# Optimization experiments

Measured on AMD Instinct MI355X. Metric: run time of the kernel, lower is better.

Reference implementation:

```python
import jax, jax.numpy as jnp
import numpy as np

B, S, D = 2, 2048, 2048
H, KVH, HD = 16, 4, 128
I = 8192
EPS = 1e-6
SCALE = HD ** -0.5
NEG = -1e9


def rms_norm(x, w):
    xf = x.astype(jnp.float32)
    var = jnp.mean(xf * xf, axis=-1, keepdims=True)
    return (w * (xf * jax.lax.rsqrt(var + EPS)).astype(x.dtype))


def rope(x, cos_f, sin_f):
    # x: (B, h, S, HD); cos_f/sin_f: (B, 1, S, HD//2). Interleaved pairs.
    xp = x.reshape(*x.shape[:-1], HD // 2, 2)
    xr, xi = xp[..., 0], xp[..., 1]
    rr = cos_f * xr - sin_f * xi
    ri = sin_f * xr + cos_f * xi
    return jnp.stack([rr, ri], axis=-1).reshape(x.shape)


def setup_inputs() -> dict:
    key = jax.random.key(0)
    ks = jax.random.split(key, 12)
    inp = {
        "hidden_states": jax.random.normal(ks[0], (B, S, D), jnp.float32),
        "cos": jax.random.normal(ks[1], (B, S, HD), jnp.float32),
        "sin": jax.random.normal(ks[2], (B, S, HD), jnp.float32),
    }
    # additive causal mask (B,1,S,S)
    causal = jnp.tril(jnp.ones((S, S), jnp.bool_))
    inp["attention_mask"] = jnp.where(causal, 0.0, NEG).astype(jnp.float32)[None, None].repeat(B, 0)
    sc = 0.02
    inp["wq"] = jax.random.normal(ks[3], (H * HD, D), jnp.float32) * sc
    inp["wk"] = jax.random.normal(ks[4], (KVH * HD, D), jnp.float32) * sc
    inp["wv"] = jax.random.normal(ks[5], (KVH * HD, D), jnp.float32) * sc
    inp["wo"] = jax.random.normal(ks[6], (D, H * HD), jnp.float32) * sc
    inp["w_gate"] = jax.random.normal(ks[7], (I, D), jnp.float32) * sc
    inp["w_up"] = jax.random.normal(ks[8], (I, D), jnp.float32) * sc
    inp["w_down"] = jax.random.normal(ks[9], (D, I), jnp.float32) * sc
    inp["ln1_w"] = jnp.ones((D,), jnp.float32)
    inp["ln2_w"] = jnp.ones((D,), jnp.float32)
    return inp


def layer_fwd(hidden_states, cos, sin, attention_mask,
              wq, wk, wv, wo, w_gate, w_up, w_down, ln1_w, ln2_w):
    residual = hidden_states
    h = rms_norm(hidden_states, ln1_w)
    # projections
    q = jnp.einsum('bsd,ed->bse', h, wq).reshape(B, S, H, HD).transpose(0, 2, 1, 3)
    k = jnp.einsum('bsd,ed->bse', h, wk).reshape(B, S, KVH, HD).transpose(0, 2, 1, 3)
    v = jnp.einsum('bsd,ed->bse', h, wv).reshape(B, S, KVH, HD).transpose(0, 2, 1, 3)
    cos_f = cos[..., :HD // 2][:, None]  # (B,1,S,HD/2)
    sin_f = sin[..., :HD // 2][:, None]
    q = rope(q, cos_f, sin_f)
    k = rope(k, cos_f, sin_f)
    # GQA: repeat_interleave kv heads
    n_rep = H // KVH
    k = jnp.repeat(k, n_rep, axis=1)
    v = jnp.repeat(v, n_rep, axis=1)
    scores = jnp.einsum('bhqd,bhkd->bhqk', q, k) * SCALE + attention_mask
    probs = jax.nn.softmax(scores.astype(jnp.float32), axis=-1).astype(q.dtype)
    attn = jnp.einsum('bhqk,bhkd->bhqd', probs, v)
    attn = attn.transpose(0, 2, 1, 3).reshape(B, S, H * HD)
    attn_out = jnp.einsum('bse,de->bsd', attn, wo)
    h = residual + attn_out
    residual = h
    m = rms_norm(h, ln2_w)
    gate = jax.nn.silu(jnp.einsum('bsd,id->bsi', m, w_gate))
    up = jnp.einsum('bsd,id->bsi', m, w_up)
    mlp_out = jnp.einsum('bsi,di->bsd', gate * up, w_down)
    return residual + mlp_out


def reference(hidden_states, cos, sin, attention_mask,
              wq, wk, wv, wo, w_gate, w_up, w_down, ln1_w, ln2_w):
    return layer_fwd(hidden_states, cos, sin, attention_mask,
                     wq, wk, wv, wo, w_gate, w_up, w_down, ln1_w, ln2_w)
```

## Files before the change

### kernel.cpp

```cpp
#include <hip/hip_runtime.h>
#include <cstdint>
#include <cstddef>

typedef unsigned short u16;
typedef short bf16x8 __attribute__((ext_vector_type(8)));
typedef float floatx4 __attribute__((ext_vector_type(4)));

__device__ __forceinline__ float b2f(u16 u) {
    union { unsigned int i; float f; } v; v.i = ((unsigned int)u) << 16; return v.f;
}
__device__ __forceinline__ u16 f2b(float f) {
    union { float f; unsigned int i; } v; v.f = f;
    unsigned int u = v.i;
    unsigned int r = (u + 0x7fffu + ((u >> 16) & 1u)) >> 16;
    return (u16)r;
}

#define GLL16(gptr, lptr)                                                          \
    __builtin_amdgcn_global_load_lds(                                              \
        (__attribute__((address_space(1))) void*)(gptr),                           \
        (__attribute__((address_space(3))) void*)(lptr), 16, 0, 0)

#define BAR_LGKM() asm volatile("s_waitcnt lgkmcnt(0)\n\ts_barrier" ::: "memory")
#define WAIT_VM8_BAR() asm volatile("s_waitcnt vmcnt(8)\n\ts_barrier" ::: "memory")
#define WAIT_VM0_BAR() asm volatile("s_waitcnt vmcnt(0)\n\ts_barrier" ::: "memory")
#define VMW(n) asm volatile("s_waitcnt vmcnt(" #n ")" ::: "memory")
#define LGKM0() asm volatile("s_waitcnt lgkmcnt(0)" ::: "memory")

__global__ __launch_bounds__(256) void cvt_all(
    const float* __restrict__ wq, const float* __restrict__ wk,
    const float* __restrict__ wvp, const float* __restrict__ wo,
    const float* __restrict__ wg, const float* __restrict__ wu,
    const float* __restrict__ wd,
    u16* __restrict__ wqkv, u16* __restrict__ wob, u16* __restrict__ wgb,
    u16* __restrict__ wub, u16* __restrict__ wdb) {
    long v = (long)blockIdx.x * 256 + threadIdx.x;
    const float* s; u16* d; long o;
    if (v < 1048576)       { s = wq;  d = wqkv;           o = v; }
    else if (v < 1310720)  { s = wk;  d = wqkv + 4194304; o = v - 1048576; }
    else if (v < 1572864)  { s = wvp; d = wqkv + 5242880; o = v - 1310720; }
    else if (v < 2621440)  { s = wo;  d = wob;            o = v - 1572864; }
    else if (v < 6815744)  { s = wg;  d = wgb;            o = v - 2621440; }
    else if (v < 11010048) { s = wu;  d = wub;            o = v - 6815744; }
    else                   { s = wd;  d = wdb;            o = v - 11010048; }
    float4 x = ((const float4*)s)[o];
    u16 t[4] = { f2b(x.x), f2b(x.y), f2b(x.z), f2b(x.w) };
    ((ushort4*)d)[o] = *(const ushort4*)t;
}

__global__ __launch_bounds__(256) void rmsnorm_kernel(const float* __restrict__ x,
                                                      const float* __restrict__ w,
                                                      u16* __restrict__ out) {
    __shared__ float red[4];
    const int row = blockIdx.x;
    const float* xr = x + (size_t)row * 2048;
    const int d0 = threadIdx.x * 8;
    float4 a = *(const float4*)&xr[d0];
    float4 b = *(const float4*)&xr[d0 + 4];
    float s = a.x*a.x + a.y*a.y + a.z*a.z + a.w*a.w +
              b.x*b.x + b.y*b.y + b.z*b.z + b.w*b.w;
    #pragma unroll
    for (int m = 1; m < 64; m <<= 1) s += __shfl_xor(s, m);
    const int lane = threadIdx.x & 63, wv = threadIdx.x >> 6;
    if (lane == 0) red[wv] = s;
    __syncthreads();
    float tot = red[0] + red[1] + red[2] + red[3];
    float r = rsqrtf(tot * (1.0f / 2048.0f) + 1e-6f);
    const float* wp = w + d0;
    u16 o[8];
    o[0] = f2b(a.x * r * wp[0]); o[1] = f2b(a.y * r * wp[1]);
    o[2] = f2b(a.z * r * wp[2]); o[3] = f2b(a.w * r * wp[3]);
    o[4] = f2b(b.x * r * wp[4]); o[5] = f2b(b.y * r * wp[5]);
    o[6] = f2b(b.z * r * wp[6]); o[7] = f2b(b.w * r * wp[7]);
    *(bf16x8*)&out[(size_t)row * 2048 + d0] = *(const bf16x8*)o;
}

__global__ __launch_bounds__(256, 2) void gemm_bt(
    const u16* __restrict__ A, const u16* __restrict__ W,
    int M, int N, int K, int mode,
    u16* __restrict__ outb, float* __restrict__ outf,
    const float* __restrict__ res) {

    __shared__ __align__(16) u16 smA[2][128 * 64];
    __shared__ __align__(16) u16 smB[2][128 * 64];

    const int tid  = threadIdx.x;
    const int lane = tid & 63;
    const int c    = lane & 15;
    const int quad = lane >> 4;
    const int wv   = tid >> 6;
    const int wm   = (wv >> 1) * 64;
    const int wn   = (wv & 1) * 64;
    const int row0 = blockIdx.y * 128;
    const int col0 = blockIdx.x * 128;

    const u16* aB[4]; const u16* bB[4]; int lo[4];
    #pragma unroll
    for (int p = 0; p < 4; ++p) {
        int lin = p * 256 + tid, r = lin >> 3, g = lin & 7, sg = g ^ (r & 7);
        aB[p] = A + (size_t)(row0 + r) * K + sg * 8;
        bB[p] = W + (size_t)(col0 + r) * K + sg * 8;
        lo[p] = lin * 8;
    }
    #pragma unroll
    for (int p = 0; p < 4; ++p) { GLL16(aB[p], &smA[0][lo[p]]); GLL16(bB[p], &smB[0][lo[p]]); }

    floatx4 acc[4][4] = {};
    const int nk = K >> 6;
    for (int k = 0; k < nk; ++k) {
        BAR_LGKM();
        if (k + 1 < nk) {
            const int nb = (k + 1) & 1, ko = (k + 1) << 6;
            #pragma unroll
            for (int p = 0; p < 4; ++p) {
                GLL16(aB[p] + ko, &smA[nb][lo[p]]);
                GLL16(bB[p] + ko, &smB[nb][lo[p]]);
            }
            WAIT_VM8_BAR();
        } else {
            WAIT_VM0_BAR();
        }
        const u16* sA = smA[k & 1];
        const u16* sB = smB[k & 1];
        #pragma unroll
        for (int ks = 0; ks < 2; ++ks) {
            bf16x8 af[4], bfr[4];
            #pragma unroll
            for (int mi = 0; mi < 4; ++mi) {
                int r = wm + mi * 16 + c;
                int pos = (ks * 4 + quad) ^ (c & 7);
                af[mi] = *(const bf16x8*)&sA[r * 64 + pos * 8];
            }
            #pragma unroll
            for (int ni = 0; ni < 4; ++ni) {
                int r = wn + ni * 16 + c;
                int pos = (ks * 4 + quad) ^ (c & 7);
                bfr[ni] = *(const bf16x8*)&sB[r * 64 + pos * 8];
            }
            #pragma unroll
            for (int mi = 0; mi < 4; ++mi)
                #pragma unroll
                for (int ni = 0; ni < 4; ++ni)
                    acc[mi][ni] = __builtin_amdgcn_mfma_f32_16x16x32_bf16(
                        af[mi], bfr[ni], acc[mi][ni], 0, 0, 0);
        }
    }

    #pragma unroll
    for (int mi = 0; mi < 4; ++mi) {
        #pragma unroll
        for (int r = 0; r < 4; ++r) {
            int row = row0 + wm + mi * 16 + quad * 4 + r;
            #pragma unroll
            for (int ni = 0; ni < 4; ++ni) {
                int col = col0 + wn + ni * 16 + c;
                size_t idx = (size_t)row * N + col;
                float v = acc[mi][ni][r];
                if (mode == 0) outb[idx] = f2b(v);
                else           outf[idx] = v + res[idx];
            }
        }
    }
}

#define STAGE_G(buf, ko) { GLL16(gSrc0 + (ko), &smG[buf][guD0]); GLL16(gSrc1 + (ko), &smG[buf][guD1]); }
#define STAGE_U(buf, ko) { GLL16(uSrc0 + (ko), &smU[buf][guD0]); GLL16(uSrc1 + (ko), &smU[buf][guD1]); }
#define STAGE_A(buf, ko, j)                                                    \
    GLL16(aSrc + (size_t)(j) * 32 * 2048 + (ko), &smA[buf][aDst + (j) * 32 * 64])

#define READ_B()                                                               \
    _Pragma("unroll")                                                          \
    for (int ks = 0; ks < 2; ++ks)                                             \
        _Pragma("unroll")                                                      \
        for (int ni = 0; ni < 2; ++ni) {                                       \
            int r = wn + ni * 16 + c;                                          \
            int pos = (ks * 4 + quad) ^ (c & 7);                               \
            bg[ni][ks] = *(const bf16x8*)&sG[r * 64 + pos * 8];                \
            bu[ni][ks] = *(const bf16x8*)&sU[r * 64 + pos * 8];                \
        }

#define MLP_PH(ph, WAITCODE, READS_EXTRA, STAGE_STMT)                          \
    {                                                                          \
        WAITCODE;                                                              \
        __builtin_amdgcn_s_barrier();                                          \
        READS_EXTRA;                                                           \
        bf16x8 af[2][2];                                                       \
        _Pragma("unroll")                                                      \
        for (int mi = 0; mi < 2; ++mi)                                         \
            _Pragma("unroll")                                                  \
            for (int ks = 0; ks < 2; ++ks) {                                   \
                int r = wm + (ph) * 32 + mi * 16 + c;                          \
                int pos = (ks * 4 + quad) ^ (c & 7);                           \
                af[mi][ks] = *(const bf16x8*)&sA[r * 64 + pos * 8];            \
            }                                                                  \
        STAGE_STMT;                                                            \
        LGKM0();                                                               \
        __builtin_amdgcn_s_setprio(1);                                         \
        _Pragma("unroll")                                                      \
        for (int mi = 0; mi < 2; ++mi)                                         \
            _Pragma("unroll")                                                  \
            for (int ks = 0; ks < 2; ++ks)                                     \
                _Pragma("unroll")                                              \
                for (int ni = 0; ni < 2; ++ni) {                               \
                    ag[(ph) * 2 + mi][ni] = __builtin_amdgcn_mfma_f32_16x16x32_bf16( \
                        af[mi][ks], bg[ni][ks], ag[(ph) * 2 + mi][ni], 0, 0, 0);     \
                    au[(ph) * 2 + mi][ni] = __builtin_amdgcn_mfma_f32_16x16x32_bf16( \
                        af[mi][ks], bu[ni][ks], au[(ph) * 2 + mi][ni], 0, 0, 0);     \
                }                                                              \
        __builtin_amdgcn_s_setprio(0);                                         \
    }

__global__ __launch_bounds__(512, 2) void mlp_gateup4(
    const u16* __restrict__ A, const u16* __restrict__ Wg,
    const u16* __restrict__ Wu, u16* __restrict__ out) {

    __shared__ __align__(16) u16 smA[2][256 * 64];
    __shared__ __align__(16) u16 smG[2][128 * 64];
    __shared__ __align__(16) u16 smU[2][128 * 64];

    const int K = 2048;
    const int tid  = threadIdx.x;
    const int lane = tid & 63;
    const int c    = lane & 15;
    const int quad = lane >> 4;
    const int wv   = tid >> 6;
    const int wm   = (wv >> 2) * 128;
    const int wn   = (wv & 3) * 32;

    const int bid  = (int)blockIdx.x;
    const int orig = (bid & 7) * 128 + (bid >> 3);
    const int row0 = (orig & 15) * 256;
    const int col0 = (orig >> 4) * 128;

    const int rloc = tid >> 3, g = tid & 7;
    const int Rbase = (tid < 256) ? rloc : (96 + rloc);
    const int sgA = g ^ (rloc & 7);
    const u16* aSrc = A + (size_t)(row0 + Rbase) * K + sgA * 8;
    const int aDst = Rbase * 64 + g * 8;

    const u16* gSrc0; const u16* gSrc1; const u16* uSrc0; const u16* uSrc1;
    int guD0, guD1;
    {
        int lin = tid, r = lin >> 3, gg = lin & 7, sg = gg ^ (r & 7);
        gSrc0 = Wg + (size_t)(col0 + r) * K + sg * 8;
        uSrc0 = Wu + (size_t)(col0 + r) * K + sg * 8;
        guD0 = lin * 8;
        lin = 512 + tid; r = lin >> 3; gg = lin & 7; sg = gg ^ (r & 7);
        gSrc1 = Wg + (size_t)(col0 + r) * K + sg * 8;
        uSrc1 = Wu + (size_t)(col0 + r) * K + sg * 8;
        guD1 = lin * 8;
    }

    STAGE_G(0, 0); STAGE_U(0, 0);
    STAGE_A(0, 0, 0); STAGE_A(0, 0, 1); STAGE_A(0, 0, 2); STAGE_A(0, 0, 3);

    floatx4 ag[8][2] = {}, au[8][2] = {};
    const int nk = K >> 6;
    for (int k = 0; k < nk; ++k) {
        const int cur = k & 1, nb = cur ^ 1;
        const int ko = (k + 1) << 6;
        const u16* sA = smA[cur];
        const u16* sG = smG[cur];
        const u16* sU = smU[cur];
        bf16x8 bg[2][2], bu[2][2];

        if (k + 1 < nk) {
            MLP_PH(0, VMW(3), READ_B(),
                   { STAGE_G(nb, ko); STAGE_U(nb, ko); STAGE_A(nb, ko, 0); });
            MLP_PH(1, VMW(7), , STAGE_A(nb, ko, 1));
            MLP_PH(2, VMW(7), , STAGE_A(nb, ko, 2));
            MLP_PH(3, VMW(7), , STAGE_A(nb, ko, 3));
        } else {
            MLP_PH(0, VMW(3), READ_B(), );
            MLP_PH(1, VMW(2), , );
            MLP_PH(2, VMW(1), , );
            MLP_PH(3, VMW(0), , );
        }
    }

    #pragma unroll
    for (int mi = 0; mi < 8; ++mi) {
        #pragma unroll
        for (int r = 0; r < 4; ++r) {
            int row = row0 + wm + mi * 16 + quad * 4 + r;
            #pragma unroll
            for (int ni = 0; ni < 2; ++ni) {
                int col = col0 + wn + ni * 16 + c;
                float gv = ag[mi][ni][r];
                float uv = au[mi][ni][r];
                float sg_ = gv / (1.0f + __expf(-gv));
                out[(size_t)row * 8192 + col] = f2b(sg_ * uv);
            }
        }
    }
}

__global__ __launch_bounds__(256) void rope_kernel(u16* __restrict__ qkv,
                                                   const float* __restrict__ cs,
                                                   const float* __restrict__ sn) {
    const int t = blockIdx.x;
    const int hh = blockIdx.y * 4 + (threadIdx.x >> 6);
    const int j = threadIdx.x & 63;
    size_t base = (size_t)t * 3072 + (hh < 16 ? hh * 128 : 2048 + (hh - 16) * 128);
    float cf = cs[(size_t)t * 128 + j];
    float sf = sn[(size_t)t * 128 + j];
    ushort2 xv = *(ushort2*)&qkv[base + 2 * j];
    float xr = b2f(xv.x), xi = b2f(xv.y);
    ushort2 ov;
    ov.x = f2b(cf * xr - sf * xi);
    ov.y = f2b(sf * xr + cf * xi);
    *(ushort2*)&qkv[base + 2 * j] = ov;
}

__global__ __launch_bounds__(256) void transpose_v(const u16* __restrict__ qkv,
                                                   u16* __restrict__ vt) {
    __shared__ __align__(16) u16 T[64][136];
    const int bkv = blockIdx.x;
    const int st = blockIdx.y;
    const int b = bkv >> 2, kvh = bkv & 3;
    const int tid = threadIdx.x;
    #pragma unroll
    for (int it = 0; it < 4; ++it) {
        int lin = it * 256 + tid;
        int sr = lin >> 4, gr = lin & 15;
        bf16x8 v = *(const bf16x8*)&qkv[((size_t)(b * 2048 + st * 64 + sr)) * 3072 +
                                        2560 + kvh * 128 + gr * 8];
        *(bf16x8*)&T[sr][gr * 8] = v;
    }
    __syncthreads();
    #pragma unroll
    for (int it = 0; it < 4; ++it) {
        int lin = it * 256 + tid;
        int n = lin >> 3, sc = lin & 7;
        u16 tmp[8];
        #pragma unroll
        for (int j = 0; j < 8; ++j) tmp[j] = T[sc * 8 + j][n];
        *(bf16x8*)&vt[((size_t)(bkv * 128 + n)) * 2048 + st * 64 + sc * 8] =
            *(const bf16x8*)tmp;
    }
}

__global__ __launch_bounds__(256, 2) void attn_kernel(const u16* __restrict__ qkv,
                                                      const u16* __restrict__ vt,
                                                      u16* __restrict__ attnb) {
    __shared__ __align__(16) u16 sK[64 * 128];
    __shared__ __align__(16) u16 sV[128 * 64];
    __shared__ __align__(16) u16 sP[4][16 * 80];

    const int tid  = threadIdx.x;
    const int lane = tid & 63;
    const int c    = lane & 15;
    const int quad = lane >> 4;
    const int wv   = tid >> 6;

    const int qt  = 31 - (int)blockIdx.x;
    const int bh  = blockIdx.y;
    const int b   = bh >> 4;
    const int h   = bh & 15;
    const int kvh = h >> 2;

    const int qrow = qt * 64 + wv * 16 + c;
    const size_t qbase = ((size_t)(b * 2048 + qrow)) * 3072 + h * 128;
    bf16x8 qf[4];
    #pragma unroll
    for (int kk = 0; kk < 4; ++kk)
        qf[kk] = *(const bf16x8*)&qkv[qbase + kk * 32 + quad * 8];

    floatx4 o[8] = {};
    float m_[4], l_[4];
    #pragma unroll
    for (int r = 0; r < 4; ++r) { m_[r] = -__builtin_inff(); l_[r] = 0.0f; }

    const float SC = 0.08838834764831845f;

    for (int kt = 0; kt <= qt; ++kt) {
        const int kv0 = kt * 64;
        __syncthreads();
        #pragma unroll
        for (int p = 0; p < 4; ++p) {
            int lin = p * 256 + tid;
            {
                int r = lin >> 4, g = lin & 15;
                int sg = g ^ (r & 7);
                const u16* gk = qkv + ((size_t)(b * 2048 + kv0 + r)) * 3072 +
                                2048 + kvh * 128 + sg * 8;
                GLL16(gk, &sK[lin * 8]);
            }
            {
                int r = lin >> 3, g = lin & 7;
                int sg = g ^ (r & 7);
                const u16* gv = vt + ((size_t)((b * 4 + kvh) * 128 + r)) * 2048 +
                                kv0 + sg * 8;
                GLL16(gv, &sV[lin * 8]);
            }
        }
        __syncthreads();

        floatx4 s[4] = {};
        #pragma unroll
        for (int kk = 0; kk < 4; ++kk) {
            #pragma unroll
            for (int ct = 0; ct < 4; ++ct) {
                int rk = ct * 16 + c;
                int pos = (kk * 4 + quad) ^ (c & 7);
                bf16x8 kf = *(const bf16x8*)&sK[rk * 128 + pos * 8];
                s[ct] = __builtin_amdgcn_mfma_f32_16x16x32_bf16(qf[kk], kf, s[ct], 0, 0, 0);
            }
        }

        const int qloc = wv * 16 + quad * 4;
        #pragma unroll
        for (int ct = 0; ct < 4; ++ct) {
            #pragma unroll
            for (int r = 0; r < 4; ++r) {
                float v = s[ct][r] * SC;
                if (kt == qt && (ct * 16 + c) > (qloc + r)) v = -__builtin_inff();
                s[ct][r] = v;
            }
        }

        float alpha[4];
        #pragma unroll
        for (int r = 0; r < 4; ++r) {
            float rm = fmaxf(fmaxf(s[0][r], s[1][r]), fmaxf(s[2][r], s[3][r]));
            rm = fmaxf(rm, __shfl_xor(rm, 1));
            rm = fmaxf(rm, __shfl_xor(rm, 2));
            rm = fmaxf(rm, __shfl_xor(rm, 4));
            rm = fmaxf(rm, __shfl_xor(rm, 8));
            float mn = fmaxf(m_[r], rm);
            alpha[r] = __expf(m_[r] - mn);
            m_[r] = mn;
        }
        #pragma unroll
        for (int r = 0; r < 4; ++r) {
            float rs = 0.0f;
            #pragma unroll
            for (int ct = 0; ct < 4; ++ct) {
                float p = __expf(s[ct][r] - m_[r]);
                s[ct][r] = p;
                rs += p;
            }
            rs += __shfl_xor(rs, 1);
            rs += __shfl_xor(rs, 2);
            rs += __shfl_xor(rs, 4);
            rs += __shfl_xor(rs, 8);
            l_[r] = l_[r] * alpha[r] + rs;
        }

        u16* sp = &sP[wv][0];
        #pragma unroll
        for (int ct = 0; ct < 4; ++ct)
            #pragma unroll
            for (int r = 0; r < 4; ++r)
                sp[(quad * 4 + r) * 80 + ct * 16 + c] = f2b(s[ct][r]);

        #pragma unroll
        for (int nt = 0; nt < 8; ++nt)
            #pragma unroll
            for (int r = 0; r < 4; ++r)
                o[nt][r] *= alpha[r];

        #pragma unroll
        for (int ks2 = 0; ks2 < 2; ++ks2) {
            bf16x8 pa = *(const bf16x8*)&sp[c * 80 + ks2 * 32 + quad * 8];
            #pragma unroll
            for (int nt = 0; nt < 8; ++nt) {
                int rv = nt * 16 + c;
                int pos = (ks2 * 4 + quad) ^ (c & 7);
                bf16x8 vb = *(const bf16x8*)&sV[rv * 64 + pos * 8];
                o[nt] = __builtin_amdgcn_mfma_f32_16x16x32_bf16(pa, vb, o[nt], 0, 0, 0);
            }
        }
    }

    float inv[4];
    #pragma unroll
    for (int r = 0; r < 4; ++r) inv[r] = 1.0f / l_[r];
    #pragma unroll
    for (int nt = 0; nt < 8; ++nt) {
        #pragma unroll
        for (int r = 0; r < 4; ++r) {
            int row = qt * 64 + wv * 16 + quad * 4 + r;
            int col = h * 128 + nt * 16 + c;
            attnb[((size_t)(b * 2048 + row)) * 2048 + col] = f2b(o[nt][r] * inv[r]);
        }
    }
}

extern "C" void kernel_launch(void* const* d_in, const int* in_sizes, int n_in,
                              void* d_out, int out_size, void* d_ws, size_t ws_size,
                              hipStream_t stream) {
    const float* hidden = (const float*)d_in[0];
    const float* cosp   = (const float*)d_in[1];
    const float* sinp   = (const float*)d_in[2];
    const float* wq  = (const float*)d_in[4];
    const float* wk  = (const float*)d_in[5];
    const float* wvp = (const float*)d_in[6];
    const float* wo  = (const float*)d_in[7];
    const float* wg  = (const float*)d_in[8];
    const float* wu  = (const float*)d_in[9];
    const float* wd  = (const float*)d_in[10];
    const float* ln1 = (const float*)d_in[11];
    const float* ln2 = (const float*)d_in[12];
    float* outp = (float*)d_out;

    char* ws = (char*)d_ws;
    size_t off = 0;
    auto alloc = [&](size_t bytes) {
        void* p = ws + off;
        off += (bytes + 255) & ~(size_t)255;
        return p;
    };
    u16* wqkv_b  = (u16*)alloc((size_t)3072 * 2048 * 2);
    u16* wo_b    = (u16*)alloc((size_t)2048 * 2048 * 2);
    u16* wg_b    = (u16*)alloc((size_t)8192 * 2048 * 2);
    u16* wu_b    = (u16*)alloc((size_t)8192 * 2048 * 2);
    u16* wd_b    = (u16*)alloc((size_t)2048 * 8192 * 2);
    u16* normed  = (u16*)alloc((size_t)4096 * 2048 * 2);
    u16* qkv     = (u16*)alloc((size_t)4096 * 3072 * 2);
    u16* vtb     = (u16*)alloc((size_t)8 * 128 * 2048 * 2);
    u16* attnb   = (u16*)alloc((size_t)4096 * 2048 * 2);
    float* h1    = (float*)alloc((size_t)4096 * 2048 * 4);
    u16* hidprod = (u16*)alloc((size_t)4096 * 8192 * 2);
    (void)ws_size; (void)in_sizes; (void)n_in; (void)out_size;

    cvt_all<<<59392, 256, 0, stream>>>(wq, wk, wvp, wo, wg, wu, wd,
                                       wqkv_b, wo_b, wg_b, wu_b, wd_b);

    rmsnorm_kernel<<<4096, 256, 0, stream>>>(hidden, ln1, normed);

    gemm_bt<<<dim3(24, 32), 256, 0, stream>>>(normed, wqkv_b, 4096, 3072, 2048, 0,
                                              qkv, nullptr, nullptr);

    rope_kernel<<<dim3(4096, 5), 256, 0, stream>>>(qkv, cosp, sinp);
    transpose_v<<<dim3(8, 32), 256, 0, stream>>>(qkv, vtb);
    attn_kernel<<<dim3(32, 32), 256, 0, stream>>>(qkv, vtb, attnb);

    gemm_bt<<<dim3(16, 32), 256, 0, stream>>>(attnb, wo_b, 4096, 2048, 2048, 1,
                                              nullptr, h1, hidden);

    rmsnorm_kernel<<<4096, 256, 0, stream>>>(h1, ln2, normed);

    mlp_gateup4<<<dim3(1024), 512, 0, stream>>>(normed, wg_b, wu_b, hidprod);

    gemm_bt<<<dim3(16, 32), 256, 0, stream>>>(hidprod, wd_b, 4096, 2048, 8192, 1,
                                              nullptr, outp, h1);
}
```

Baseline: 1.068 ms.

## Software-pipeline LDS fragment reads ahead of MFMAs in gate/up MLP kernel

Restructures the fused gate/up GEMM main loop so the A fragments for the next phase and the B fragments for the next k-step are read from LDS while the current phase's MFMAs issue. Explicit lgkmcnt waits before each MFMA block go away, and the barrier is merged with the vmcnt wait. The aim is to hide LDS read latency and cut stalls between the four phases of each k-step. In exchange it holds more live fragment registers (double A buffers plus next B fragments), which could pressure occupancy at 512 threads x 2 blocks. It also relies on subtle barrier ordering against buffer reuse.

```diff
diff --git a/kernel.cpp b/kernel.cpp
--- a/kernel.cpp
+++ b/kernel.cpp
@@ -24,8 +24,8 @@
 #define BAR_LGKM() asm volatile("s_waitcnt lgkmcnt(0)\n\ts_barrier" ::: "memory")
 #define WAIT_VM8_BAR() asm volatile("s_waitcnt vmcnt(8)\n\ts_barrier" ::: "memory")
 #define WAIT_VM0_BAR() asm volatile("s_waitcnt vmcnt(0)\n\ts_barrier" ::: "memory")
-#define VMW(n) asm volatile("s_waitcnt vmcnt(" #n ")" ::: "memory")
-#define LGKM0() asm volatile("s_waitcnt lgkmcnt(0)" ::: "memory")
+#define WAITV_BAR(n) asm volatile("s_waitcnt vmcnt(" #n ")\n\ts_barrier" ::: "memory")
+#define BAR_ONLY() asm volatile("s_barrier" ::: "memory")
 
 __global__ __launch_bounds__(256) void cvt_all(
     const float* __restrict__ wq, const float* __restrict__ wk,
@@ -163,54 +163,50 @@
     }
 }
 
-#define STAGE_G(buf, ko) { GLL16(gSrc0 + (ko), &smG[buf][guD0]); GLL16(gSrc1 + (ko), &smG[buf][guD1]); }
-#define STAGE_U(buf, ko) { GLL16(uSrc0 + (ko), &smU[buf][guD0]); GLL16(uSrc1 + (ko), &smU[buf][guD1]); }
-#define STAGE_A(buf, ko, j)                                                    \
+#define STAGE_A1u(buf, ko, j)                                                  \
     GLL16(aSrc + (size_t)(j) * 32 * 2048 + (ko), &smA[buf][aDst + (j) * 32 * 64])
-
-#define READ_B()                                                               \
+#define STAGE_HEAD(buf, ko) {                                                  \
+    GLL16(gSrc0 + (ko), &smG[buf][guD0]); GLL16(gSrc1 + (ko), &smG[buf][guD1]);\
+    GLL16(uSrc0 + (ko), &smU[buf][guD0]); GLL16(uSrc1 + (ko), &smU[buf][guD1]);\
+    STAGE_A1u(buf, ko, 0); }
+
+#define READ_AF(dst, sAp, p)                                                   \
+    _Pragma("unroll")                                                          \
+    for (int mi = 0; mi < 2; ++mi)                                             \
+        _Pragma("unroll")                                                      \
+        for (int ks = 0; ks < 2; ++ks) {                                       \
+            int r = wm + (p) * 32 + mi * 16 + c;                               \
+            int pos = (ks * 4 + quad) ^ (c & 7);                               \
+            dst[mi][ks] = *(const bf16x8*)&(sAp)[r * 64 + pos * 8];            \
+        }
+
+#define READ_B2(bgv, buv, sGp, sUp)                                            \
     _Pragma("unroll")                                                          \
     for (int ks = 0; ks < 2; ++ks)                                             \
         _Pragma("unroll")                                                      \
         for (int ni = 0; ni < 2; ++ni) {                                       \
             int r = wn + ni * 16 + c;                                          \
             int pos = (ks * 4 + quad) ^ (c & 7);                               \
-            bg[ni][ks] = *(const bf16x8*)&sG[r * 64 + pos * 8];                \
-            bu[ni][ks] = *(const bf16x8*)&sU[r * 64 + pos * 8];                \
-        }
-
-#define MLP_PH(ph, WAITCODE, READS_EXTRA, STAGE_STMT)                          \
-    {                                                                          \
-        WAITCODE;                                                              \
-        __builtin_amdgcn_s_barrier();                                          \
-        READS_EXTRA;                                                           \
-        bf16x8 af[2][2];                                                       \
+            bgv[ni][ks] = *(const bf16x8*)&(sGp)[r * 64 + pos * 8];            \
+            buv[ni][ks] = *(const bf16x8*)&(sUp)[r * 64 + pos * 8];            \
+        }
+
+#define MFMA16(p, afv)                                                         \
+    __builtin_amdgcn_s_setprio(1);                                             \
+    _Pragma("unroll")                                                          \
+    for (int mi = 0; mi < 2; ++mi)                                             \
         _Pragma("unroll")                                                      \
-        for (int mi = 0; mi < 2; ++mi)                                         \
+        for (int ks = 0; ks < 2; ++ks)                                         \
             _Pragma("unroll")                                                  \
-            for (int ks = 0; ks < 2; ++ks) {                                   \
-                int r = wm + (ph) * 32 + mi * 16 + c;                          \
-                int pos = (ks * 4 + quad) ^ (c & 7);                           \
-                af[mi][ks] = *(const bf16x8*)&sA[r * 64 + pos * 8];            \
+            for (int ni = 0; ni < 2; ++ni) {                                   \
+                ag[(p) * 2 + mi][ni] = __builtin_amdgcn_mfma_f32_16x16x32_bf16(\
+                    afv[mi][ks], bg[ni][ks], ag[(p) * 2 + mi][ni], 0, 0, 0);   \
+                au[(p) * 2 + mi][ni] = __builtin_amdgcn_mfma_f32_16x16x32_bf16(\
+                    afv[mi][ks], bu[ni][ks], au[(p) * 2 + mi][ni], 0, 0, 0);   \
             }                                                                  \
-        STAGE_STMT;                                                            \
-        LGKM0();                                                               \
-        __builtin_amdgcn_s_setprio(1);                                         \
-        _Pragma("unroll")                                                      \
-        for (int mi = 0; mi < 2; ++mi)                                         \
-            _Pragma("unroll")                                                  \
-            for (int ks = 0; ks < 2; ++ks)                                     \
-                _Pragma("unroll")                                              \
-                for (int ni = 0; ni < 2; ++ni) {                               \
-                    ag[(ph) * 2 + mi][ni] = __builtin_amdgcn_mfma_f32_16x16x32_bf16( \
-                        af[mi][ks], bg[ni][ks], ag[(ph) * 2 + mi][ni], 0, 0, 0);     \
-                    au[(ph) * 2 + mi][ni] = __builtin_amdgcn_mfma_f32_16x16x32_bf16( \
-                        af[mi][ks], bu[ni][ks], au[(ph) * 2 + mi][ni], 0, 0, 0);     \
-                }                                                              \
-        __builtin_amdgcn_s_setprio(0);                                         \
-    }
-
-__global__ __launch_bounds__(512, 2) void mlp_gateup4(
+    __builtin_amdgcn_s_setprio(0);
+
+__global__ __launch_bounds__(512, 2) void mlp_gateup5(
     const u16* __restrict__ A, const u16* __restrict__ Wg,
     const u16* __restrict__ Wu, u16* __restrict__ out) {
 
@@ -251,31 +247,52 @@
         guD1 = lin * 8;
     }
 
-    STAGE_G(0, 0); STAGE_U(0, 0);
-    STAGE_A(0, 0, 0); STAGE_A(0, 0, 1); STAGE_A(0, 0, 2); STAGE_A(0, 0, 3);
+    STAGE_HEAD(0, 0);
+    STAGE_A1u(0, 0, 1); STAGE_A1u(0, 0, 2); STAGE_A1u(0, 0, 3);
+    WAITV_BAR(2);
+    bf16x8 bg[2][2], bu[2][2], afA[2][2], afB[2][2];
+    READ_B2(bg, bu, smG[0], smU[0]);
+    READ_AF(afA, smA[0], 0);
 
     floatx4 ag[8][2] = {}, au[8][2] = {};
-    const int nk = K >> 6;
-    for (int k = 0; k < nk; ++k) {
+    for (int k = 0; k < 31; ++k) {
         const int cur = k & 1, nb = cur ^ 1;
         const int ko = (k + 1) << 6;
         const u16* sA = smA[cur];
-        const u16* sG = smG[cur];
-        const u16* sU = smU[cur];
-        bf16x8 bg[2][2], bu[2][2];
-
-        if (k + 1 < nk) {
-            MLP_PH(0, VMW(3), READ_B(),
-                   { STAGE_G(nb, ko); STAGE_U(nb, ko); STAGE_A(nb, ko, 0); });
-            MLP_PH(1, VMW(7), , STAGE_A(nb, ko, 1));
-            MLP_PH(2, VMW(7), , STAGE_A(nb, ko, 2));
-            MLP_PH(3, VMW(7), , STAGE_A(nb, ko, 3));
-        } else {
-            MLP_PH(0, VMW(3), READ_B(), );
-            MLP_PH(1, VMW(2), , );
-            MLP_PH(2, VMW(1), , );
-            MLP_PH(3, VMW(0), , );
-        }
+        STAGE_HEAD(nb, ko);
+        READ_AF(afB, sA, 1);
+        MFMA16(0, afA);
+        WAITV_BAR(6);
+        STAGE_A1u(nb, ko, 1);
+        READ_AF(afA, sA, 2);
+        MFMA16(1, afB);
+        WAITV_BAR(6);
+        STAGE_A1u(nb, ko, 2);
+        READ_AF(afB, sA, 3);
+        MFMA16(2, afA);
+        WAITV_BAR(2);
+        STAGE_A1u(nb, ko, 3);
+        bf16x8 bgn[2][2], bun[2][2];
+        READ_B2(bgn, bun, smG[nb], smU[nb]);
+        READ_AF(afA, smA[nb], 0);
+        MFMA16(3, afB);
+        WAITV_BAR(2);
+        #pragma unroll
+        for (int ks = 0; ks < 2; ++ks)
+            #pragma unroll
+            for (int ni = 0; ni < 2; ++ni) { bg[ni][ks] = bgn[ni][ks]; bu[ni][ks] = bun[ni][ks]; }
+    }
+    {
+        const u16* sA = smA[1];
+        READ_AF(afB, sA, 1);
+        MFMA16(0, afA);
+        WAITV_BAR(1);
+        READ_AF(afA, sA, 2);
+        MFMA16(1, afB);
+        WAITV_BAR(0);
+        READ_AF(afB, sA, 3);
+        MFMA16(2, afA);
+        MFMA16(3, afB);
     }
 
     #pragma unroll
@@ -541,7 +558,7 @@
 
     rmsnorm_kernel<<<4096, 256, 0, stream>>>(h1, ln2, normed);
 
-    mlp_gateup4<<<dim3(1024), 512, 0, stream>>>(normed, wg_b, wu_b, hidprod);
+    mlp_gateup5<<<dim3(1024), 512, 0, stream>>>(normed, wg_b, wu_b, hidprod);
 
     gemm_bt<<<dim3(16, 32), 256, 0, stream>>>(hidprod, wd_b, 4096, 2048, 8192, 1,
                                               nullptr, outp, h1);
```

After: 1.207 ms. 13.0% more time.

## Double-buffer K/V tiles in attention kernel and raise MFMA wave priority

Applied to the files above, without the earlier changes.

The attention kernel now keeps two LDS buffers for K and V and prefetches the next tile with global_load_lds while the current tile is being computed. Partial vmcnt waits replace the full syncthreads round-trips. Global addresses are precomputed once per thread, and s_setprio raises wave priority around the MFMA loops. The second buffer doubles K/V LDS use to about 74KB per block, which may limit occupancy under the 2-blocks-per-CU launch bound. Attention is only part of the whole layer's time.

```diff
diff --git a/kernel.cpp b/kernel.cpp
--- a/kernel.cpp
+++ b/kernel.cpp
@@ -24,6 +24,7 @@
 #define BAR_LGKM() asm volatile("s_waitcnt lgkmcnt(0)\n\ts_barrier" ::: "memory")
 #define WAIT_VM8_BAR() asm volatile("s_waitcnt vmcnt(8)\n\ts_barrier" ::: "memory")
 #define WAIT_VM0_BAR() asm volatile("s_waitcnt vmcnt(0)\n\ts_barrier" ::: "memory")
+#define WAITV_BAR(n) asm volatile("s_waitcnt vmcnt(" #n ")\n\ts_barrier" ::: "memory")
 #define VMW(n) asm volatile("s_waitcnt vmcnt(" #n ")" ::: "memory")
 #define LGKM0() asm volatile("s_waitcnt lgkmcnt(0)" ::: "memory")
 
@@ -340,11 +341,20 @@
     }
 }
 
+#define ATTN_STAGE(bufi, kt_) {                                                \
+    const size_t koK = (size_t)(kt_) * 64 * 3072;                              \
+    const int    koV = (kt_) * 64;                                             \
+    _Pragma("unroll")                                                          \
+    for (int p = 0; p < 4; ++p) {                                              \
+        GLL16(gkB[p] + koK, &sK[bufi][lK[p]]);                                 \
+        GLL16(gvB[p] + koV, &sV[bufi][lV[p]]);                                 \
+    } }
+
 __global__ __launch_bounds__(256, 2) void attn_kernel(const u16* __restrict__ qkv,
                                                       const u16* __restrict__ vt,
                                                       u16* __restrict__ attnb) {
-    __shared__ __align__(16) u16 sK[64 * 128];
-    __shared__ __align__(16) u16 sV[128 * 64];
+    __shared__ __align__(16) u16 sK[2][64 * 128];
+    __shared__ __align__(16) u16 sV[2][128 * 64];
     __shared__ __align__(16) u16 sP[4][16 * 80];
 
     const int tid  = threadIdx.x;
@@ -359,6 +369,18 @@
     const int h   = bh & 15;
     const int kvh = h >> 2;
 
+    const u16* gkB[4]; const u16* gvB[4]; int lK[4], lV[4];
+    #pragma unroll
+    for (int p = 0; p < 4; ++p) {
+        int lin = p * 256 + tid;
+        { int r = lin >> 4, g = lin & 15, sg = g ^ (r & 7);
+          gkB[p] = qkv + ((size_t)(b * 2048 + r)) * 3072 + 2048 + kvh * 128 + sg * 8;
+          lK[p] = lin * 8; }
+        { int r = lin >> 3, g = lin & 7, sg = g ^ (r & 7);
+          gvB[p] = vt + ((size_t)((b * 4 + kvh) * 128 + r)) * 2048 + sg * 8;
+          lV[p] = lin * 8; }
+    }
+
     const int qrow = qt * 64 + wv * 16 + c;
     const size_t qbase = ((size_t)(b * 2048 + qrow)) * 3072 + h * 128;
     bf16x8 qf[4];
@@ -373,40 +395,27 @@
 
     const float SC = 0.08838834764831845f;
 
+    ATTN_STAGE(0, 0);
+
     for (int kt = 0; kt <= qt; ++kt) {
-        const int kv0 = kt * 64;
-        __syncthreads();
-        #pragma unroll
-        for (int p = 0; p < 4; ++p) {
-            int lin = p * 256 + tid;
-            {
-                int r = lin >> 4, g = lin & 15;
-                int sg = g ^ (r & 7);
-                const u16* gk = qkv + ((size_t)(b * 2048 + kv0 + r)) * 3072 +
-                                2048 + kvh * 128 + sg * 8;
-                GLL16(gk, &sK[lin * 8]);
-            }
-            {
-                int r = lin >> 3, g = lin & 7;
-                int sg = g ^ (r & 7);
-                const u16* gv = vt + ((size_t)((b * 4 + kvh) * 128 + r)) * 2048 +
-                                kv0 + sg * 8;
-                GLL16(gv, &sV[lin * 8]);
-            }
-        }
-        __syncthreads();
+        const int cur = kt & 1, nb = cur ^ 1;
+        BAR_LGKM();
+        if (kt < qt) { ATTN_STAGE(nb, kt + 1); WAIT_VM8_BAR(); }
+        else         { WAIT_VM0_BAR(); }
 
         floatx4 s[4] = {};
+        __builtin_amdgcn_s_setprio(1);
         #pragma unroll
         for (int kk = 0; kk < 4; ++kk) {
             #pragma unroll
             for (int ct = 0; ct < 4; ++ct) {
                 int rk = ct * 16 + c;
                 int pos = (kk * 4 + quad) ^ (c & 7);
-                bf16x8 kf = *(const bf16x8*)&sK[rk * 128 + pos * 8];
+                bf16x8 kf = *(const bf16x8*)&sK[cur][rk * 128 + pos * 8];
                 s[ct] = __builtin_amdgcn_mfma_f32_16x16x32_bf16(qf[kk], kf, s[ct], 0, 0, 0);
             }
         }
+        __builtin_amdgcn_s_setprio(0);
 
         const int qloc = wv * 16 + quad * 4;
         #pragma unroll
@@ -460,6 +469,7 @@
             for (int r = 0; r < 4; ++r)
                 o[nt][r] *= alpha[r];
 
+        __builtin_amdgcn_s_setprio(1);
         #pragma unroll
         for (int ks2 = 0; ks2 < 2; ++ks2) {
             bf16x8 pa = *(const bf16x8*)&sp[c * 80 + ks2 * 32 + quad * 8];
@@ -467,10 +477,11 @@
             for (int nt = 0; nt < 8; ++nt) {
                 int rv = nt * 16 + c;
                 int pos = (ks2 * 4 + quad) ^ (c & 7);
-                bf16x8 vb = *(const bf16x8*)&sV[rv * 64 + pos * 8];
+                bf16x8 vb = *(const bf16x8*)&sV[cur][rv * 64 + pos * 8];
                 o[nt] = __builtin_amdgcn_mfma_f32_16x16x32_bf16(pa, vb, o[nt], 0, 0, 0);
             }
         }
+        __builtin_amdgcn_s_setprio(0);
     }
 
     float inv[4];
```

Result: no change. 1.051 ms (-1.6%).
